# Optimization experiments

Hardware: AMD Instinct MI355X
Metric: run time of the kernel (lower is better)

## Reference

```python
import jax, jax.numpy as jnp
import numpy as np

DECAY = 0.99
EPS = 1e-5  # Laplace smoothing eps in cluster-size balancing


def _quantize(z_flat, embedding, cluster_size, emb_avg, n_codes):
    # z_flat: [N, D]; embedding: [K, D]
    d = (jnp.sum(z_flat * z_flat, axis=1, keepdims=True)
         + jnp.sum(embedding * embedding, axis=1)
         - 2.0 * (z_flat @ embedding.T))                      # [N, K]
    idx = jnp.argmin(d, axis=1)                               # [N]
    # EMA update (training path). segment_sum == one-hot matmul scatter-add.
    counts = jax.ops.segment_sum(jnp.ones(z_flat.shape[0], z_flat.dtype), idx,
                                 num_segments=n_codes)        # [K]
    new_cs = cluster_size * DECAY + (1.0 - DECAY) * counts
    dw = jax.ops.segment_sum(z_flat, idx, num_segments=n_codes)  # [K, D]
    new_avg = emb_avg * DECAY + (1.0 - DECAY) * dw
    n = new_cs.sum()
    bal = (new_cs + EPS) / (n + n_codes * EPS) * n
    # torch assigns via .data (no autograd) -> stop_gradient for faithfulness
    new_emb = jax.lax.stop_gradient(new_avg / bal[:, None])
    z_q = jnp.take(new_emb, idx, axis=0)  # == one_hot(idx) @ new_emb
    return idx, z_q


def _l2norm(x):
    # F.normalize(x, dim=-1) with eps=1e-12
    return x / jnp.maximum(jnp.linalg.norm(x, axis=-1, keepdims=True), 1e-12)


def reference(z, structure_embedding, style_embedding,
              structure_cluster_size, style_cluster_size,
              structure_embedding_avg, style_embedding_avg):
    b, c, h, w, d = z.shape
    zp = jnp.transpose(z, (0, 2, 3, 4, 1))      # b h w d c
    z_flat = zp.reshape(-1, c)                  # [N, D]
    s_idx, s_q = _quantize(z_flat, structure_embedding, structure_cluster_size,
                           structure_embedding_avg, structure_embedding.shape[0])
    y_idx, y_q = _quantize(z_flat, style_embedding, style_cluster_size,
                           style_embedding_avg, style_embedding.shape[0])

    def back(q):  # [N, C] -> b c h w d
        return jnp.transpose(q.reshape(b, h, w, d, c), (0, 4, 1, 2, 3))

    s_enc = back(s_q)
    y_enc = back(y_q)
    # NOTE: faithful to source — normalize over LAST axis of (b,c,h,w,d),
    # i.e. the spatial depth axis, exactly as F.normalize(dim=-1) does there.
    dis = jnp.mean(jnp.sum(_l2norm(s_enc) * _l2norm(y_enc), axis=-1) ** 2)
    z_q = (s_enc + y_enc) * 0.5
    return z_q, dis, s_idx, y_idx


def setup_inputs() -> dict:
    key = jax.random.key(0)
    k1, k2, k3 = jax.random.split(key, 3)
    B, C, H, W, D = 16, 256, 16, 16, 16
    Ks, Ky = 1024, 512
    return {
        "z": jax.random.normal(k1, (B, C, H, W, D), dtype=jnp.float32),
        "structure_embedding": jax.random.normal(k2, (Ks, C), dtype=jnp.float32),
        "style_embedding": jax.random.normal(k3, (Ky, C), dtype=jnp.float32),
        "structure_cluster_size": jnp.zeros((Ks,), jnp.float32),
        "style_cluster_size": jnp.zeros((Ky,), jnp.float32),
        "structure_embedding_avg": jnp.zeros((Ks, C), jnp.float32),
        "style_embedding_avg": jnp.zeros((Ky, C), jnp.float32),
    }
```

## Files before the change

kernel.cpp:

```cpp
#include <hip/hip_runtime.h>
#include <float.h>

#define NROWS 65536
#define CDIM  256
#define KS    1024
#define KY    512
#define KTOT  1536
#define SPB   4096

#define WB_CNT_S       0
#define WB_CNT_Y       4096
#define WB_RESCUE_CNT  6144
#define WB_DISACC      6152
#define WB_DW_S        6400
#define WB_DW_Y        1054976
#define WB_ZERO_BYTES  1579264
#define WB_EIMG        1579264
#define WB_EN2         2365696
#define WB_IDXS_I      2371840
#define WB_IDXY_I      2633984
#define WB_RLIST_S     2896128
#define WB_RLIST_Y     3158272
#define WB_BASE_S      3420416
#define WB_BASE_Y      3424512
#define WB_CUR_S       3426560
#define WB_CUR_Y       3430656
#define WB_SCALE_S     3432704
#define WB_SCALE_Y     3436800
#define WB_PERM_S      3438848
#define WB_PERM_Y      3700992
#define WB_KSORT_S     3963136
#define WB_KSORT_Y     4225280
#define WB_EMB_S       4487424
#define WB_EMB_Y       5536000

#define OFF_OUT_ZQ   0
#define OFF_OUT_DIS  16777216
#define OFF_OUT_SIDX 16777217
#define OFF_OUT_YIDX 16842753

typedef __attribute__((ext_vector_type(8)))  _Float16 f16x8;
typedef __attribute__((ext_vector_type(4)))  float    f32x4;

__device__ __forceinline__ unsigned int umn(unsigned int a, unsigned int b) { return a < b ? a : b; }
__device__ __forceinline__ unsigned int umx(unsigned int a, unsigned int b) { return a > b ? a : b; }

__global__ void prep_e(const float* __restrict__ Es, const float* __restrict__ Ey,
                       unsigned short* __restrict__ eimg, float* __restrict__ en2) {
    int k = blockIdx.x;
    int lane = threadIdx.x;
    const float* E = (k < KS) ? (Es + (size_t)k * CDIM) : (Ey + (size_t)(k - KS) * CDIM);
    float4 v = *(const float4*)(E + lane * 4);
    float nrm = v.x * v.x + v.y * v.y + v.z * v.z + v.w * v.w;
#pragma unroll
    for (int off = 32; off > 0; off >>= 1) nrm += __shfl_down(nrm, off);
    if (lane == 0) en2[k] = nrm;

    unsigned short q0 = __builtin_bit_cast(unsigned short, (_Float16)v.x);
    unsigned short q1 = __builtin_bit_cast(unsigned short, (_Float16)v.y);
    unsigned short q2 = __builtin_bit_cast(unsigned short, (_Float16)v.z);
    unsigned short q3 = __builtin_bit_cast(unsigned short, (_Float16)v.w);
    uint2 hp = make_uint2((unsigned)q0 | ((unsigned)q1 << 16),
                          (unsigned)q2 | ((unsigned)q3 << 16));

    int c0 = lane * 4;
    int kc = c0 >> 5, g = (c0 >> 3) & 3, j0 = c0 & 7;
    size_t byteoff = (size_t)(k >> 4) * 8192 + (size_t)kc * 1024
                   + (size_t)(g * 16 + (k & 15)) * 16 + (size_t)j0 * 2;
    *(uint2*)((char*)eimg + byteoff) = hp;
}

__global__ void prep_z(const float* __restrict__ z, float* __restrict__ zf) {
    __shared__ float Zs[32][257];
    int blk = blockIdx.x;
    int n0 = blk * 32, b = n0 >> 12, s0 = n0 & 4095;
    int t = threadIdx.x;
    const float* zb = z + (size_t)b * CDIM * SPB + s0;
#pragma unroll
    for (int i = 0; i < 32; ++i) {
        int l = i * 256 + t;
        int c = l >> 5, s = l & 31;
        Zs[s][c] = zb[(size_t)c * SPB + s];
    }
    __syncthreads();
#pragma unroll
    for (int j = 0; j < 8; ++j) {
        int gid = j * 256 + t;
        int nl = gid >> 6, fg = gid & 63;
        float4 v = *(const float4*)(&Zs[nl][fg * 4]);
        *(float4*)(&zf[(size_t)(n0 + nl) * 256 + fg * 4]) = v;
    }
}

__device__ __forceinline__ void stage1(const unsigned short* __restrict__ eimg,
                                       int chunk, char* lds, int wave, int lane) {
    const char* gs = (const char*)eimg + (size_t)chunk * 8192 + wave * 2048 + lane * 16;
    char* ls = lds + wave * 2048;
    __builtin_amdgcn_global_load_lds(
        (const __attribute__((address_space(1))) void*)gs,
        (__attribute__((address_space(3))) void*)ls, 16, 0, 0);
    __builtin_amdgcn_global_load_lds(
        (const __attribute__((address_space(1))) void*)(gs + 1024),
        (__attribute__((address_space(3))) void*)(ls + 1024), 16, 0, 0);
}

#define WAITV(n)                                                               \
    asm volatile("s_waitcnt vmcnt(" #n ")");                                   \
    __builtin_amdgcn_sched_barrier(0);

#define PSFLUSH(dst)                                                           \
    {                                                                          \
        _Pragma("unroll")                                                      \
        for (int rg = 0; rg < 2; ++rg)                                         \
        _Pragma("unroll")                                                      \
        for (int q = 0; q < 4; ++q) {                                          \
            unsigned int v1 = m1a[rg][q], v2 = m2a[rg][q];                     \
            _Pragma("unroll")                                                  \
            for (int m = 8; m >= 1; m >>= 1) {                                 \
                unsigned int o1 = (unsigned int)__shfl_xor((int)v1, m);        \
                unsigned int o2 = (unsigned int)__shfl_xor((int)v2, m);        \
                v2 = umn(umn(v2, o2), umx(v1, o1));                            \
                v1 = umn(v1, o1);                                              \
            }                                                                  \
            if ((lane & 15) == 0) {                                            \
                int n = n0 + rg * 16 + (lane >> 4) * 4 + q;                    \
                dst[n] = make_uint2(v1, v2);                                   \
            }                                                                  \
            m1a[rg][q] = 0xFFFFFFFFu; m2a[rg][q] = 0xFFFFFFFFu;                \
        }                                                                      \
    }

#define FLUSHY()                                                               \
    {                                                                          \
        _Pragma("unroll")                                                      \
        for (int rg = 0; rg < 2; ++rg)                                         \
        _Pragma("unroll")                                                      \
        for (int q = 0; q < 4; ++q) {                                          \
            unsigned int v1 = m1a[rg][q], v2 = m2a[rg][q];                     \
            _Pragma("unroll")                                                  \
            for (int m = 8; m >= 1; m >>= 1) {                                 \
                unsigned int o1 = (unsigned int)__shfl_xor((int)v1, m);        \
                unsigned int o2 = (unsigned int)__shfl_xor((int)v2, m);        \
                v2 = umn(umn(v2, o2), umx(v1, o1));                            \
                v1 = umn(v1, o1);                                              \
            }                                                                  \
            if ((lane & 15) == 0) {                                            \
                int kw = (int)(v1 & 0x7FFu) - KS;                              \
                int n = n0 + rg * 16 + (lane >> 4) * 4 + q;                    \
                yidx_f[n] = (float)kw;                                         \
                yidx_i[n] = kw;                                                \
                atomicAdd(&cnt_y[kw], 1);                                      \
                if ((v1 >> 11) + 4 > (v2 >> 11)) {                             \
                    int k2w = (int)(v2 & 0x7FFu) - KS;                         \
                    int pp = atomicAdd(&rescue_cnt[1], 1);                     \
                    if (pp < 65536) rlist_y[pp] = n | (k2w << 16);             \
                }                                                              \
            }                                                                  \
        }                                                                      \
    }

__launch_bounds__(256, 4)
__global__ void assign_kernel(const float* __restrict__ zf, const unsigned short* __restrict__ eimg,
                              const float* __restrict__ en2g,
                              uint2* __restrict__ ps0, uint2* __restrict__ ps1,
                              float* __restrict__ yidx_f, int* __restrict__ yidx_i,
                              int* __restrict__ cnt_y, int* __restrict__ rescue_cnt,
                              int* __restrict__ rlist_y) {
    __shared__ char  sh[4][8192];
    __shared__ float en2l[KTOT];
    const int tid = threadIdx.x, wave = tid >> 6, lane = tid & 63;
    const int half = blockIdx.x & 1;
    const int n0 = (blockIdx.x >> 1) * 128 + wave * 32;
    const int cb = half * 48;

    for (int i = tid; i < KTOT; i += 256) en2l[i] = en2g[i];

    f16x8 A[2][8];
#pragma unroll
    for (int rg = 0; rg < 2; ++rg) {
        const float* zr = zf + (size_t)(n0 + rg * 16 + (lane & 15)) * 256 + (lane >> 4) * 8;
#pragma unroll
        for (int kc = 0; kc < 8; ++kc) {
            float4 f0 = *(const float4*)(zr + kc * 32);
            float4 f1 = *(const float4*)(zr + kc * 32 + 4);
            f16x8 a;
            a[0] = (_Float16)f0.x; a[1] = (_Float16)f0.y;
            a[2] = (_Float16)f0.z; a[3] = (_Float16)f0.w;
            a[4] = (_Float16)f1.x; a[5] = (_Float16)f1.y;
            a[6] = (_Float16)f1.z; a[7] = (_Float16)f1.w;
            A[rg][kc] = a;
        }
    }

    unsigned int m1a[2][4], m2a[2][4];
#pragma unroll
    for (int rg = 0; rg < 2; ++rg)
#pragma unroll
        for (int q = 0; q < 4; ++q) { m1a[rg][q] = 0xFFFFFFFFu; m2a[rg][q] = 0xFFFFFFFFu; }

    stage1(eimg, cb + 0, &sh[0][0], wave, lane);
    stage1(eimg, cb + 1, &sh[1][0], wave, lane);
    stage1(eimg, cb + 2, &sh[2][0], wave, lane);
    __syncthreads();

#pragma unroll 1
    for (int i = 0; i < 48; ++i) {
        if (i < 46)       { WAITV(4); }
        else if (i == 46) { WAITV(2); }
        else              { WAITV(0); }
        __builtin_amdgcn_s_barrier();
        asm volatile("" ::: "memory");
        if (i + 3 < 48) stage1(eimg, cb + i + 3, &sh[(i + 3) & 3][0], wave, lane);

        const int chunk = cb + i;
        const char* bb = &sh[i & 3][0] + lane * 16;
        f32x4 acc0 = {}, acc1 = {};
#pragma unroll
        for (int kc = 0; kc < 8; ++kc) {
            f16x8 B = *(const f16x8*)(bb + kc * 1024);
            acc0 = __builtin_amdgcn_mfma_f32_16x16x32_f16(A[0][kc], B, acc0, 0, 0, 0);
            acc1 = __builtin_amdgcn_mfma_f32_16x16x32_f16(A[1][kc], B, acc1, 0, 0, 0);
        }
        const int kcode = chunk * 16 + (lane & 15);
        const float en0 = en2l[kcode] + 512.0f;
        const unsigned int tag = (unsigned int)kcode;
#pragma unroll
        for (int q = 0; q < 4; ++q) {
            float d0 = fmaf(-2.f, acc0[q], en0);
            unsigned int du0 = (__float_as_uint(d0) & 0xFFFFF800u) | tag;
            m2a[0][q] = umn(m2a[0][q], umx(m1a[0][q], du0));
            m1a[0][q] = umn(m1a[0][q], du0);
            float d1 = fmaf(-2.f, acc1[q], en0);
            unsigned int du1 = (__float_as_uint(d1) & 0xFFFFF800u) | tag;
            m2a[1][q] = umn(m2a[1][q], umx(m1a[1][q], du1));
            m1a[1][q] = umn(m1a[1][q], du1);
        }

        if (half == 1 && i == 15) PSFLUSH(ps1);
    }

    if (half == 0) { PSFLUSH(ps0); }
    else           { FLUSHY(); }
}

__global__ void merge_s_kernel(const uint2* __restrict__ ps0, const uint2* __restrict__ ps1,
                               float* __restrict__ sidx_f, int* __restrict__ sidx_i,
                               int* __restrict__ cnt_s, int* __restrict__ rescue_cnt,
                               int* __restrict__ rlist_s) {
    int n = blockIdx.x * 256 + threadIdx.x;
    uint2 a = ps0[n], b = ps1[n];
    unsigned int v1 = umn(a.x, b.x);
    unsigned int v2 = umn(umn(a.y, b.y), umx(a.x, b.x));
    int kw = (int)(v1 & 0x7FFu);
    sidx_f[n] = (float)kw;
    sidx_i[n] = kw;
    atomicAdd(&cnt_s[kw], 1);
    if ((v1 >> 11) + 4 > (v2 >> 11)) {
        int k2w = (int)(v2 & 0x7FFu);
        int pp = atomicAdd(&rescue_cnt[0], 1);
        if (pp < 65536) rlist_s[pp] = n | (k2w << 16);
    }
}

__global__ void rescue2_kernel(const float* __restrict__ zf,
                               const float* __restrict__ Es, const float* __restrict__ Ey,
                               const float* __restrict__ en2, const int* __restrict__ rcnt,
                               const int* __restrict__ rlist_s, const int* __restrict__ rlist_y,
                               float* __restrict__ sidx_f, float* __restrict__ yidx_f,
                               int* __restrict__ sidx_i, int* __restrict__ yidx_i,
                               int* __restrict__ cnt_s, int* __restrict__ cnt_y) {
    int cs = rcnt[0]; if (cs > 65536) cs = 65536;
    int cy = rcnt[1]; if (cy > 65536) cy = 65536;
    int total = cs + cy;
    const int lane = threadIdx.x & 63;
    const int nw = (gridDim.x * blockDim.x) >> 6;
    for (int e = (int)((blockIdx.x * blockDim.x + threadIdx.x) >> 6); e < total; e += nw) {
        int book = (e >= cs);
        unsigned int ent = (unsigned int)(book ? rlist_y[e - cs] : rlist_s[e]);
        int n  = (int)(ent & 0xFFFFu);
        int k2 = (int)(ent >> 16);
        int* idx_i = book ? yidx_i : sidx_i;
        float* idx_f = book ? yidx_f : sidx_f;
        int* cnt = book ? cnt_y : cnt_s;
        const float* E = book ? Ey : Es;
        const float* en2k = book ? (en2 + KS) : en2;
        int k1 = idx_i[n];
        float4 zv = *(const float4*)(zf + (size_t)n * 256 + lane * 4);
        float4 a  = *(const float4*)(E + (size_t)k1 * 256 + lane * 4);
        float4 c  = *(const float4*)(E + (size_t)k2 * 256 + lane * 4);
        float d1 = zv.x * a.x + zv.y * a.y + zv.z * a.z + zv.w * a.w;
        float d2 = zv.x * c.x + zv.y * c.y + zv.z * c.z + zv.w * c.w;
#pragma unroll
        for (int off = 32; off > 0; off >>= 1) {
            d1 += __shfl_down(d1, off);
            d2 += __shfl_down(d2, off);
        }
        if (lane == 0) {
            float dist1 = en2k[k1] - 2.f * d1;
            float dist2 = en2k[k2] - 2.f * d2;
            int nk = (dist2 < dist1 || (dist2 == dist1 && k2 < k1)) ? k2 : k1;
            if (nk != k1) {
                atomicSub(&cnt[k1], 1);
                atomicAdd(&cnt[nk], 1);
                idx_i[n] = nk;
                idx_f[n] = (float)nk;
            }
        }
    }
}

__global__ void scanbal_kernel(const float* __restrict__ cs_in, const float* __restrict__ cy_in,
                               const int* __restrict__ cnt_s, const int* __restrict__ cnt_y,
                               int* __restrict__ base_s, int* __restrict__ base_y,
                               int* __restrict__ cur_s, int* __restrict__ cur_y,
                               float* __restrict__ scale_s, float* __restrict__ scale_y) {
    __shared__ int   sc[1024];
    __shared__ float sf[1024];
    int K = blockIdx.x ? KY : KS;
    const float* csi = blockIdx.x ? cy_in : cs_in;
    const int*   cnt = blockIdx.x ? cnt_y : cnt_s;
    int* base = blockIdx.x ? base_y : base_s;
    int* cur  = blockIdx.x ? cur_y  : cur_s;
    float* scale = blockIdx.x ? scale_y : scale_s;
    int t = threadIdx.x;
    int c = (t < K) ? cnt[t] : 0;
    float ncs = (t < K) ? (csi[t] * 0.99f + 0.01f * (float)c) : 0.f;
    sc[t] = c;
    __syncthreads();
    for (int off = 1; off < 1024; off <<= 1) {
        int v = sc[t] + ((t >= off) ? sc[t - off] : 0);
        __syncthreads();
        sc[t] = v;
        __syncthreads();
    }
    int incl = sc[t];
    sf[t] = ncs;
    __syncthreads();
    for (int s2 = 512; s2 > 0; s2 >>= 1) {
        if (t < s2) sf[t] += sf[t + s2];
        __syncthreads();
    }
    float nsum = sf[0];
    if (t < K) {
        base[t] = incl - c;
        cur[t]  = incl - c;
        float bal = (ncs + 1e-5f) / (nsum + (float)K * 1e-5f) * nsum;
        scale[t] = 1.0f / bal;
    }
}

__global__ void scatter_kernel(const int* __restrict__ si, const int* __restrict__ yi,
                               int* __restrict__ cur_s, int* __restrict__ cur_y,
                               int* __restrict__ perm_s, int* __restrict__ perm_y,
                               int* __restrict__ ksort_s, int* __restrict__ ksort_y) {
    int i = blockIdx.x * 256 + threadIdx.x;
    if (i < NROWS) {
        int k = si[i]; int p = atomicAdd(&cur_s[k], 1);
        perm_s[p] = i; ksort_s[p] = k;
    } else {
        int n = i - NROWS; int k = yi[n]; int p = atomicAdd(&cur_y[k], 1);
        perm_y[p] = n; ksort_y[p] = k;
    }
}

__global__ void dw_kernel(const float* __restrict__ zf,
                          const int* __restrict__ perm_s, const int* __restrict__ ksort_s,
                          const int* __restrict__ perm_y, const int* __restrict__ ksort_y,
                          float* __restrict__ dw_s, float* __restrict__ dw_y) {
    __shared__ int keys[33];
    __shared__ int rows[32];
    const int t = threadIdx.x;
    int blk = blockIdx.x;
    const int* perm; const int* ks; float* dw; int p0;
    if (blk < NROWS / 32) { perm = perm_s; ks = ksort_s; dw = dw_s; p0 = blk * 32; }
    else                  { perm = perm_y; ks = ksort_y; dw = dw_y; p0 = (blk - NROWS / 32) * 32; }
    if (t < 32) { keys[t] = ks[p0 + t]; rows[t] = perm[p0 + t]; }
    if (t == 32) keys[32] = -1;
    __syncthreads();
    float acc = 0.f;
#pragma unroll 8
    for (int j = 0; j < 32; ++j) {
        acc += zf[(size_t)rows[j] * 256 + t];
        if (keys[j + 1] != keys[j]) {
            atomicAdd(&dw[(size_t)keys[j] * 256 + t], acc);
            acc = 0.f;
        }
    }
}

__global__ void embnew_kernel(const float* __restrict__ avg_s, const float* __restrict__ avg_y,
                              const float* __restrict__ dw_s, const float* __restrict__ dw_y,
                              const float* __restrict__ scale_s, const float* __restrict__ scale_y,
                              float* __restrict__ emb_s, float* __restrict__ emb_y) {
    int id = blockIdx.x, t = threadIdx.x;
    if (id < KS) { int i = id * 256 + t; emb_s[i] = (avg_s[i] * 0.99f + 0.01f * dw_s[i]) * scale_s[id]; }
    else { int kk = id - KS; int i = kk * 256 + t; emb_y[i] = (avg_y[i] * 0.99f + 0.01f * dw_y[i]) * scale_y[kk]; }
}

__global__ void gather_kernel(const float* __restrict__ Se, const float* __restrict__ Ye,
                              const int* __restrict__ sidx, const int* __restrict__ yidx,
                              float* __restrict__ zq, float* __restrict__ disacc) {
    __shared__ float qb[256 * 17];
    __shared__ int   si[16], yi[16];
    __shared__ float red[256];
    const int g  = blockIdx.x;
    const int b  = g >> 8;
    const int hw = g & 255;
    const int t  = threadIdx.x;
    if (t < 16) {
        int n = b * SPB + hw * 16 + t;
        si[t] = sidx[n];
        yi[t] = yidx[n];
    }
    __syncthreads();
    float ns = 0.f, ny = 0.f, dot = 0.f;
#pragma unroll
    for (int d = 0; d < 16; ++d) {
        float s = Se[(size_t)si[d] * CDIM + t];
        float y = Ye[(size_t)yi[d] * CDIM + t];
        ns  = fmaf(s, s, ns);
        ny  = fmaf(y, y, ny);
        dot = fmaf(s, y, dot);
        qb[t * 17 + d] = 0.5f * (s + y);
    }
    float den = fmaxf(sqrtf(ns), 1e-12f) * fmaxf(sqrtf(ny), 1e-12f);
    float val = dot / den;
    red[t] = val * val;
    __syncthreads();
    for (int s = 128; s > 0; s >>= 1) {
        if (t < s) red[t] += red[t + s];
        __syncthreads();
    }
    if (t == 0) atomicAdd(disacc, red[0]);
    float* zg = zq + (size_t)b * CDIM * SPB + hw * 16;
#pragma unroll
    for (int j = 0; j < 16; ++j) {
        int e = j * 256 + t;
        int c = e >> 4, d = e & 15;
        zg[(size_t)c * SPB + d] = qb[c * 17 + d];
    }
}

__global__ void fin_kernel(const float* __restrict__ disacc, float* __restrict__ out_dis) {
    *out_dis = *disacc * (1.0f / 1048576.0f);
}

extern "C" void kernel_launch(void* const* d_in, const int* in_sizes, int n_in,
                              void* d_out, int out_size, void* d_ws, size_t ws_size,
                              hipStream_t stream) {
    const float* z     = (const float*)d_in[0];
    const float* Es    = (const float*)d_in[1];
    const float* Ey    = (const float*)d_in[2];
    const float* s_cs  = (const float*)d_in[3];
    const float* y_cs  = (const float*)d_in[4];
    const float* s_avg = (const float*)d_in[5];
    const float* y_avg = (const float*)d_in[6];
    float* out = (float*)d_out;
    char*  w   = (char*)d_ws;

    unsigned short* eimg = (unsigned short*)(w + WB_EIMG);
    float* en2    = (float*)(w + WB_EN2);
    int* idxs_i   = (int*)(w + WB_IDXS_I);
    int* idxy_i   = (int*)(w + WB_IDXY_I);
    int* cnt_s    = (int*)(w + WB_CNT_S);
    int* cnt_y    = (int*)(w + WB_CNT_Y);
    int* r_cnt    = (int*)(w + WB_RESCUE_CNT);
    int* rlist_s  = (int*)(w + WB_RLIST_S);
    int* rlist_y  = (int*)(w + WB_RLIST_Y);
    int* base_s   = (int*)(w + WB_BASE_S);
    int* base_y   = (int*)(w + WB_BASE_Y);
    int* cur_s    = (int*)(w + WB_CUR_S);
    int* cur_y    = (int*)(w + WB_CUR_Y);
    float* scale_s = (float*)(w + WB_SCALE_S);
    float* scale_y = (float*)(w + WB_SCALE_Y);
    int* perm_s   = (int*)(w + WB_PERM_S);
    int* perm_y   = (int*)(w + WB_PERM_Y);
    int* ksort_s  = (int*)(w + WB_KSORT_S);
    int* ksort_y  = (int*)(w + WB_KSORT_Y);
    float* dw_s   = (float*)(w + WB_DW_S);
    float* dw_y   = (float*)(w + WB_DW_Y);
    float* emb_s  = (float*)(w + WB_EMB_S);
    float* emb_y  = (float*)(w + WB_EMB_Y);
    uint2* ps0 = (uint2*)(w + WB_EMB_S);
    uint2* ps1 = ps0 + NROWS;

    float* zf     = out + OFF_OUT_ZQ;
    float* sidx_f = out + OFF_OUT_SIDX;
    float* yidx_f = out + OFF_OUT_YIDX;

    hipMemsetAsync(w, 0, WB_ZERO_BYTES, stream);

    prep_e<<<KTOT, 64, 0, stream>>>(Es, Ey, eimg, en2);
    prep_z<<<NROWS / 32, 256, 0, stream>>>(z, zf);

    assign_kernel<<<(NROWS / 128) * 2, 256, 0, stream>>>(
        zf, eimg, en2, ps0, ps1, yidx_f, idxy_i, cnt_y, r_cnt, rlist_y);

    merge_s_kernel<<<NROWS / 256, 256, 0, stream>>>(ps0, ps1, sidx_f, idxs_i,
                                                    cnt_s, r_cnt, rlist_s);

    rescue2_kernel<<<512, 256, 0, stream>>>(zf, Es, Ey, en2, r_cnt, rlist_s, rlist_y,
                                            sidx_f, yidx_f, idxs_i, idxy_i, cnt_s, cnt_y);

    scanbal_kernel<<<2, 1024, 0, stream>>>(s_cs, y_cs, cnt_s, cnt_y, base_s, base_y,
                                           cur_s, cur_y, scale_s, scale_y);
    scatter_kernel<<<2 * NROWS / 256, 256, 0, stream>>>(idxs_i, idxy_i, cur_s, cur_y,
                                                        perm_s, perm_y, ksort_s, ksort_y);
    dw_kernel<<<2 * NROWS / 32, 256, 0, stream>>>(zf, perm_s, ksort_s, perm_y, ksort_y, dw_s, dw_y);
    embnew_kernel<<<KTOT, 256, 0, stream>>>(s_avg, y_avg, dw_s, dw_y, scale_s, scale_y, emb_s, emb_y);
    gather_kernel<<<4096, 256, 0, stream>>>(emb_s, emb_y, idxs_i, idxy_i,
                                            out + OFF_OUT_ZQ, (float*)(w + WB_DISACC));
    fin_kernel<<<1, 1, 0, stream>>>((float*)(w + WB_DISACC), out + OFF_OUT_DIS);
}
```

Baseline: 342.9 us.

## Merge prep kernels, rotate codebook chunk order per block, raise MFMA priority

The two preprocessing kernels are merged into one launch: the first 384 blocks convert the codebooks to fp16 and compute their norms, and the remaining blocks transpose z. In the assign kernel, each block now walks its codebook chunks in a rotated order chosen by block index, while keeping the split between the structure-only and style segments. The aim is to stop concurrent blocks from all hitting the same chunks at once. The MFMA loop is wrapped in s_setprio to favour compute waves. Merging the kernels saves one launch, but the codebook blocks and the z-transpose blocks now share one grid.

```diff
diff --git a/kernel.cpp b/kernel.cpp
--- a/kernel.cpp
+++ b/kernel.cpp
@@ -45,50 +45,51 @@
 __device__ __forceinline__ unsigned int umn(unsigned int a, unsigned int b) { return a < b ? a : b; }
 __device__ __forceinline__ unsigned int umx(unsigned int a, unsigned int b) { return a > b ? a : b; }
 
-__global__ void prep_e(const float* __restrict__ Es, const float* __restrict__ Ey,
-                       unsigned short* __restrict__ eimg, float* __restrict__ en2) {
-    int k = blockIdx.x;
-    int lane = threadIdx.x;
-    const float* E = (k < KS) ? (Es + (size_t)k * CDIM) : (Ey + (size_t)(k - KS) * CDIM);
-    float4 v = *(const float4*)(E + lane * 4);
-    float nrm = v.x * v.x + v.y * v.y + v.z * v.z + v.w * v.w;
-#pragma unroll
-    for (int off = 32; off > 0; off >>= 1) nrm += __shfl_down(nrm, off);
-    if (lane == 0) en2[k] = nrm;
-
-    unsigned short q0 = __builtin_bit_cast(unsigned short, (_Float16)v.x);
-    unsigned short q1 = __builtin_bit_cast(unsigned short, (_Float16)v.y);
-    unsigned short q2 = __builtin_bit_cast(unsigned short, (_Float16)v.z);
-    unsigned short q3 = __builtin_bit_cast(unsigned short, (_Float16)v.w);
-    uint2 hp = make_uint2((unsigned)q0 | ((unsigned)q1 << 16),
-                          (unsigned)q2 | ((unsigned)q3 << 16));
-
-    int c0 = lane * 4;
-    int kc = c0 >> 5, g = (c0 >> 3) & 3, j0 = c0 & 7;
-    size_t byteoff = (size_t)(k >> 4) * 8192 + (size_t)kc * 1024
-                   + (size_t)(g * 16 + (k & 15)) * 16 + (size_t)j0 * 2;
-    *(uint2*)((char*)eimg + byteoff) = hp;
-}
-
-__global__ void prep_z(const float* __restrict__ z, float* __restrict__ zf) {
-    __shared__ float Zs[32][257];
-    int blk = blockIdx.x;
-    int n0 = blk * 32, b = n0 >> 12, s0 = n0 & 4095;
-    int t = threadIdx.x;
-    const float* zb = z + (size_t)b * CDIM * SPB + s0;
-#pragma unroll
-    for (int i = 0; i < 32; ++i) {
-        int l = i * 256 + t;
-        int c = l >> 5, s = l & 31;
-        Zs[s][c] = zb[(size_t)c * SPB + s];
-    }
-    __syncthreads();
-#pragma unroll
-    for (int j = 0; j < 8; ++j) {
-        int gid = j * 256 + t;
-        int nl = gid >> 6, fg = gid & 63;
-        float4 v = *(const float4*)(&Zs[nl][fg * 4]);
-        *(float4*)(&zf[(size_t)(n0 + nl) * 256 + fg * 4]) = v;
+__global__ void prep_kernel(const float* __restrict__ Es, const float* __restrict__ Ey,
+                            const float* __restrict__ z,
+                            unsigned short* __restrict__ eimg, float* __restrict__ en2,
+                            float* __restrict__ zf) {
+    if (blockIdx.x < 384) {
+        int wave = threadIdx.x >> 6, lane = threadIdx.x & 63;
+        int k = blockIdx.x * 4 + wave;
+        const float* E = (k < KS) ? (Es + (size_t)k * CDIM) : (Ey + (size_t)(k - KS) * CDIM);
+        float4 v = *(const float4*)(E + lane * 4);
+        float nrm = v.x * v.x + v.y * v.y + v.z * v.z + v.w * v.w;
+#pragma unroll
+        for (int off = 32; off > 0; off >>= 1) nrm += __shfl_down(nrm, off);
+        if (lane == 0) en2[k] = nrm;
+
+        unsigned short q0 = __builtin_bit_cast(unsigned short, (_Float16)v.x);
+        unsigned short q1 = __builtin_bit_cast(unsigned short, (_Float16)v.y);
+        unsigned short q2 = __builtin_bit_cast(unsigned short, (_Float16)v.z);
+        unsigned short q3 = __builtin_bit_cast(unsigned short, (_Float16)v.w);
+        uint2 hp = make_uint2((unsigned)q0 | ((unsigned)q1 << 16),
+                              (unsigned)q2 | ((unsigned)q3 << 16));
+        int c0 = lane * 4;
+        int kc = c0 >> 5, g = (c0 >> 3) & 3, j0 = c0 & 7;
+        size_t byteoff = (size_t)(k >> 4) * 8192 + (size_t)kc * 1024
+                       + (size_t)(g * 16 + (k & 15)) * 16 + (size_t)j0 * 2;
+        *(uint2*)((char*)eimg + byteoff) = hp;
+    } else {
+        __shared__ float Zs[32][257];
+        int blk = blockIdx.x - 384;
+        int n0 = blk * 32, b = n0 >> 12, s0 = n0 & 4095;
+        int t = threadIdx.x;
+        const float* zb = z + (size_t)b * CDIM * SPB + s0;
+#pragma unroll
+        for (int i = 0; i < 32; ++i) {
+            int l = i * 256 + t;
+            int c = l >> 5, s = l & 31;
+            Zs[s][c] = zb[(size_t)c * SPB + s];
+        }
+        __syncthreads();
+#pragma unroll
+        for (int j = 0; j < 8; ++j) {
+            int gid = j * 256 + t;
+            int nl = gid >> 6, fg = gid & 63;
+            float4 v = *(const float4*)(&Zs[nl][fg * 4]);
+            *(float4*)(&zf[(size_t)(n0 + nl) * 256 + fg * 4]) = v;
+        }
     }
 }
 
@@ -107,6 +108,12 @@
 #define WAITV(n)                                                               \
     asm volatile("s_waitcnt vmcnt(" #n ")");                                   \
     __builtin_amdgcn_sched_barrier(0);
+
+__device__ __forceinline__ int seqf(int i, int half, int r) {
+    if (half == 0) { int j = i + r * 12; return (j >= 48) ? j - 48 : j; }
+    if (i < 16) return 48 + ((i + r * 4) & 15);
+    return 64 + ((i - 16 + r * 8) & 31);
+}
 
 #define PSFLUSH(dst)                                                           \
     {                                                                          \
@@ -170,8 +177,8 @@
     __shared__ float en2l[KTOT];
     const int tid = threadIdx.x, wave = tid >> 6, lane = tid & 63;
     const int half = blockIdx.x & 1;
+    const int rot  = (blockIdx.x >> 1) & 3;
     const int n0 = (blockIdx.x >> 1) * 128 + wave * 32;
-    const int cb = half * 48;
 
     for (int i = tid; i < KTOT; i += 256) en2l[i] = en2g[i];
 
@@ -198,9 +205,9 @@
 #pragma unroll
         for (int q = 0; q < 4; ++q) { m1a[rg][q] = 0xFFFFFFFFu; m2a[rg][q] = 0xFFFFFFFFu; }
 
-    stage1(eimg, cb + 0, &sh[0][0], wave, lane);
-    stage1(eimg, cb + 1, &sh[1][0], wave, lane);
-    stage1(eimg, cb + 2, &sh[2][0], wave, lane);
+    stage1(eimg, seqf(0, half, rot), &sh[0][0], wave, lane);
+    stage1(eimg, seqf(1, half, rot), &sh[1][0], wave, lane);
+    stage1(eimg, seqf(2, half, rot), &sh[2][0], wave, lane);
     __syncthreads();
 
 #pragma unroll 1
@@ -210,17 +217,19 @@
         else              { WAITV(0); }
         __builtin_amdgcn_s_barrier();
         asm volatile("" ::: "memory");
-        if (i + 3 < 48) stage1(eimg, cb + i + 3, &sh[(i + 3) & 3][0], wave, lane);
-
-        const int chunk = cb + i;
+        if (i + 3 < 48) stage1(eimg, seqf(i + 3, half, rot), &sh[(i + 3) & 3][0], wave, lane);
+
+        const int chunk = seqf(i, half, rot);
         const char* bb = &sh[i & 3][0] + lane * 16;
         f32x4 acc0 = {}, acc1 = {};
+        __builtin_amdgcn_s_setprio(1);
 #pragma unroll
         for (int kc = 0; kc < 8; ++kc) {
             f16x8 B = *(const f16x8*)(bb + kc * 1024);
             acc0 = __builtin_amdgcn_mfma_f32_16x16x32_f16(A[0][kc], B, acc0, 0, 0, 0);
             acc1 = __builtin_amdgcn_mfma_f32_16x16x32_f16(A[1][kc], B, acc1, 0, 0, 0);
         }
+        __builtin_amdgcn_s_setprio(0);
         const int kcode = chunk * 16 + (lane & 15);
         const float en0 = en2l[kcode] + 512.0f;
         const unsigned int tag = (unsigned int)kcode;
@@ -490,8 +499,7 @@
 
     hipMemsetAsync(w, 0, WB_ZERO_BYTES, stream);
 
-    prep_e<<<KTOT, 64, 0, stream>>>(Es, Ey, eimg, en2);
-    prep_z<<<NROWS / 32, 256, 0, stream>>>(z, zf);
+    prep_kernel<<<384 + NROWS / 32, 256, 0, stream>>>(Es, Ey, z, eimg, en2, zf);
 
     assign_kernel<<<(NROWS / 128) * 2, 256, 0, stream>>>(
         zf, eimg, en2, ps0, ps1, yidx_f, idxy_i, cnt_y, r_cnt, rlist_y);
```

Result: slower. 350.8 us (+2.3%).
